# Kernel tuning notes

Measured on AMD Instinct MI355X. Metric: run time of the kernel, lower is better.

## Reference

```python
import jax, jax.numpy as jnp
import numpy as np

ALPHA = 0.5  # mixing weight between dot-product and wedge-norm terms


def setup_inputs() -> dict:
    key = jax.random.key(0)
    kq, kk, kv = jax.random.split(key, 3)
    B, L, H, E = 2, 2048, 8, 32
    queries = jax.random.normal(kq, (B, L, H, E), dtype=jnp.float32)
    keys = jax.random.normal(kk, (B, L, H, E), dtype=jnp.float32)
    values = jax.random.normal(kv, (B, L, H, E), dtype=jnp.float32)
    return {"queries": queries, "keys": keys, "values": values}


def reference(queries, keys, values):
    # queries: [B,L,H,E], keys: [B,S,H,E], values: [B,S,H,D]
    E = queries.shape[-1]
    scale = 1.0 / jnp.sqrt(jnp.asarray(E, dtype=queries.dtype))
    # dot product scores: [B,H,L,S]
    dot = jnp.einsum('blhe,bshe->bhls', queries, keys)
    # squared norms -> broadcastable [B,H,L,1] and [B,H,1,S]
    qn2 = jnp.sum(queries ** 2, axis=-1).transpose(0, 2, 1)[..., :, None]
    kn2 = jnp.sum(keys ** 2, axis=-1).transpose(0, 2, 1)[..., None, :]
    # wedge (Clifford) squared norm, clamped at 0
    wedge = jax.nn.relu(qn2 * kn2 - dot ** 2)
    scores = (ALPHA * dot - (1.0 - ALPHA) * wedge) * scale
    attn = jax.nn.softmax(scores, axis=-1)  # [B,H,L,S]
    # out: [B,L,H,D]
    out = jnp.einsum('bhls,bshd->blhd', attn, values)
    return out
```

## Files before the change

### kernel.cpp

```cpp
#include <hip/hip_runtime.h>
#include <hip/hip_bf16.h>
#include <math.h>


#define NB 2
#define NL 2048
#define NS 2048
#define NH 8
#define NBH 16
#define STRIPS 2
#define NT 16
#define CSC 0.12751742f
#define DEFER_THR 24.0f

#define WS_KN2_OFF 0u
#define WS_KHKL_OFF 131072u
#define WS_VT_OFF (131072u + 4194304u)
#define WS_PACC_OFF (131072u + 4194304u + 2097152u)
#define WS_PML_OFF (WS_PACC_OFF + 8388608u)
#define WS_NEED (WS_PML_OFF + 524288u)

typedef float f32x4 __attribute__((ext_vector_type(4)));
typedef float f32x2 __attribute__((ext_vector_type(2)));
typedef short s16x8 __attribute__((ext_vector_type(8)));
typedef unsigned short u16;

__device__ inline unsigned pk2(float a, float b) {
    __hip_bfloat162 t = __float22bfloat162_rn(make_float2(a, b));
    union { __hip_bfloat162 h; unsigned u; } cv;
    cv.h = t;
    return cv.u;
}
template <int CTRL>
__device__ inline float dpp_add(float x) {
    return x + __int_as_float(__builtin_amdgcn_mov_dpp(__float_as_int(x), CTRL, 0xF, 0xF, false));
}
__device__ inline void dma16(const void* gp, void* lp) {
    __builtin_amdgcn_global_load_lds(
        (__attribute__((address_space(1))) void*)(void*)gp,
        (__attribute__((address_space(3))) void*)lp, 16, 0, 0);
}
__device__ inline void pl32(unsigned& a, unsigned& b) {
    asm("v_permlane32_swap_b32 %0, %1" : "+v"(a), "+v"(b));
}
__device__ inline void pl16(unsigned& a, unsigned& b) {
    asm("v_permlane16_swap_b32 %0, %1" : "+v"(a), "+v"(b));
}
__device__ inline int swzK(int row) { return (row ^ (row >> 2)) & 3; }
__device__ inline int swzV(int row) { return (row + (row >> 3)) & 7; }

__global__ __launch_bounds__(256) void ga_pre(const float* __restrict__ K,
                                              const float* __restrict__ V,
                                              float* __restrict__ kn2w,
                                              u16* __restrict__ khkl,
                                              u16* __restrict__ vtw) {
    __shared__ float Vf[64][36];
    const int T = threadIdx.x;
    const int bh = blockIdx.x >> 5, stile = blockIdx.x & 31;
    const int b = bh >> 3, h = bh & 7;
    const int s0 = stile * 64;
    const int sk = T >> 2, kc = T & 3;

    const float* kp = K + ((size_t)((b * NS + s0 + sk) * NH + h)) * 32 + kc * 8;
    float4 f0 = *(const float4*)kp, f1 = *(const float4*)(kp + 4);
    float kx[8] = {f0.x, f0.y, f0.z, f0.w, f1.x, f1.y, f1.z, f1.w};
    unsigned hh[4], ll[4];
    float kn2p = 0.f;
#pragma unroll
    for (int i = 0; i < 4; i++) {
        float x0 = kx[2 * i], x1 = kx[2 * i + 1];
        kn2p = fmaf(x0, x0, kn2p);
        kn2p = fmaf(x1, x1, kn2p);
        unsigned h01 = pk2(x0, x1);
        hh[i] = h01;
        float h0 = __uint_as_float(h01 << 16);
        float h1 = __uint_as_float(h01 & 0xffff0000u);
        ll[i] = pk2(x0 - h0, x1 - h1);
    }
    u16* kd = khkl + ((size_t)(bh * NS + s0 + sk)) * 64;
    const int swk = sk & 7;
    *(uint4*)(kd + ((kc ^ swk) * 8)) = make_uint4(hh[0], hh[1], hh[2], hh[3]);
    *(uint4*)(kd + (((4 + kc) ^ swk) * 8)) = make_uint4(ll[0], ll[1], ll[2], ll[3]);
    kn2p = dpp_add<0xB1>(kn2p);
    kn2p = dpp_add<0x4E>(kn2p);
    if (kc == 0) kn2w[bh * NS + s0 + sk] = kn2p;

    const float* vp = V + ((size_t)((b * NS + s0 + sk) * NH + h)) * 32 + kc * 8;
    float4 g0 = *(const float4*)vp, g1 = *(const float4*)(vp + 4);
    const int chv = kc ^ ((sk >> 3) & 3);
    *(float4*)&Vf[sk][chv * 8] = g0;
    *(float4*)&Vf[sk][chv * 8 + 4] = g1;
    __syncthreads();
    const int dr = T >> 3, c = T & 7;
    float vv[8];
#pragma unroll
    for (int i = 0; i < 8; i++)
        vv[i] = Vf[c * 8 + i][(((dr >> 3) ^ (c & 3)) << 3) + (dr & 7)];
    const int phys = c ^ (dr & 7);
    *(uint4*)(vtw + ((size_t)(bh * 32 + dr)) * NS + s0 + phys * 8) =
        make_uint4(pk2(vv[0], vv[1]), pk2(vv[2], vv[3]), pk2(vv[4], vv[5]), pk2(vv[6], vv[7]));
}

__global__ __launch_bounds__(256, 3) void ga_dma(
    const float* __restrict__ Q, const float* __restrict__ kn2w,
    const u16* __restrict__ khkl, const u16* __restrict__ vtw,
    float* __restrict__ pacc, float* __restrict__ pml) {
    __shared__ u16 sK[2][64][64];
    __shared__ u16 sV[2][32][64];

    const int T = threadIdx.x;
    const int lane = T & 63, wave = T >> 6;
    const int g = lane >> 4, lc = lane & 15, g8 = g * 8;
    const int blk = blockIdx.x;
    const int qt = blk & 31, strip = (blk >> 5) & 1, bh = blk >> 6;
    const int b = bh >> 3, h = bh & 7;
    const int qw = qt * 64 + wave * 16;
    const int kb0 = strip * 1024;

    const float* qrow = Q + ((size_t)((b * NL + qw + lc) * NH + h)) * 32 + g8;
    float4 qa = *(const float4*)qrow, qb = *(const float4*)(qrow + 4);
    float q8[8] = {qa.x, qa.y, qa.z, qa.w, qb.x, qb.y, qb.z, qb.w};
    union { unsigned u4[4]; s16x8 v; } qh_, ql_;
    float qn2 = 0.f;
#pragma unroll
    for (int i = 0; i < 4; i++) {
        float x0 = q8[2 * i], x1 = q8[2 * i + 1];
        qn2 = fmaf(x0, x0, qn2);
        qn2 = fmaf(x1, x1, qn2);
        unsigned h01 = pk2(x0, x1);
        qh_.u4[i] = h01;
        float h0 = __uint_as_float(h01 << 16);
        float h1 = __uint_as_float(h01 & 0xffff0000u);
        ql_.u4[i] = pk2(x0 - h0, x1 - h1);
    }
    const s16x8 qh = qh_.v, ql = ql_.v;
    qn2 += __shfl_xor(qn2, 16);
    qn2 += __shfl_xor(qn2, 32);

    const char* ksrc = (const char*)khkl +
        ((size_t)(bh * NS + kb0 + 16 * wave)) * 128 + lane * 16;
    const char* vsrc = (const char*)vtw +
        ((size_t)(bh * 32 + 8 * wave + (lane >> 3))) * (NS * 2) +
        (size_t)(kb0 + (lane & 7) * 8) * 2;
    const float* kn2b = kn2w + (size_t)bh * NS + kb0;

    dma16(ksrc, &sK[0][16 * wave][0]);
    dma16(ksrc + 1024, &sK[0][16 * wave + 8][0]);
    dma16(vsrc, &sV[0][8 * wave][0]);
    __syncthreads();

    s16x8 ones;
#pragma unroll
    for (int i = 0; i < 8; i++) ones[i] = (short)0x3F80;

    f32x4 acc0 = {0.f, 0.f, 0.f, 0.f}, acc1 = {0.f, 0.f, 0.f, 0.f};
    f32x4 lacc = {0.f, 0.f, 0.f, 0.f};
    float m = -1e30f;
    const f32x4 z = {0.f, 0.f, 0.f, 0.f};
    const int sw = lc & 7;

    f32x4 d_p[4], kn2_p[4];
    s16x8 va_p[4];

    auto frags_qk = [&](int buf, f32x4* dc) {
#pragma unroll
        for (int st = 0; st < 4; st++) {
            s16x8 kh = *(s16x8*)&sK[buf][16 * st + lc][(g ^ sw) * 8];
            s16x8 klo = *(s16x8*)&sK[buf][16 * st + lc][((4 + g) ^ sw) * 8];
            f32x4 dd = __builtin_amdgcn_mfma_f32_16x16x32_bf16(klo, qh, z, 0, 0, 0);
            dd = __builtin_amdgcn_mfma_f32_16x16x32_bf16(kh, ql, dd, 0, 0, 0);
            dd = __builtin_amdgcn_mfma_f32_16x16x32_bf16(kh, qh, dd, 0, 0, 0);
            dc[st] = dd;
        }
    };
    auto load_v = [&](int buf, s16x8* va) {
        va[0] = *(s16x8*)&sV[buf][lc][(g ^ sw) * 8];
        va[1] = *(s16x8*)&sV[buf][lc][((4 + g) ^ sw) * 8];
        va[2] = *(s16x8*)&sV[buf][lc + 16][(g ^ sw) * 8];
        va[3] = *(s16x8*)&sV[buf][lc + 16][((4 + g) ^ sw) * 8];
    };
    auto softmax_pv = [&](const f32x4* dp, const f32x4* kn2p, const s16x8* vap) {
        const f32x2 qn2v = {qn2, qn2};
        float sc[4][4];
#pragma unroll
        for (int st = 0; st < 4; st++) {
            f32x2 dd0 = {dp[st][0], dp[st][1]}, dd1 = {dp[st][2], dp[st][3]};
            f32x2 kk0 = {kn2p[st][0], kn2p[st][1]}, kk1 = {kn2p[st][2], kn2p[st][3]};
            f32x2 e0 = dd0 - qn2v * kk0;
            f32x2 e1 = dd1 - qn2v * kk1;
            f32x2 t0 = dd0 * dd0 + e0;
            f32x2 t1 = dd1 * dd1 + e1;
            sc[st][0] = fminf(dp[st][0], t0[0]);
            sc[st][1] = fminf(dp[st][1], t0[1]);
            sc[st][2] = fminf(dp[st][2], t1[0]);
            sc[st][3] = fminf(dp[st][3], t1[1]);
        }
        float a0 = fmaxf(fmaxf(sc[0][0], sc[0][1]), sc[0][2]);
        float a1 = fmaxf(fmaxf(sc[0][3], sc[1][0]), sc[1][1]);
        float a2 = fmaxf(fmaxf(sc[1][2], sc[1][3]), sc[2][0]);
        float a3 = fmaxf(fmaxf(sc[2][1], sc[2][2]), sc[2][3]);
        float a4 = fmaxf(fmaxf(sc[3][0], sc[3][1]), sc[3][2]);
        float tm = fmaxf(fmaxf(fmaxf(a0, a1), fmaxf(a2, a3)), fmaxf(a4, sc[3][3]));
        if (!__all(tm <= m + DEFER_THR)) {
            tm = fmaxf(tm, __shfl_xor(tm, 16));
            tm = fmaxf(tm, __shfl_xor(tm, 32));
            const float nm = fmaxf(m, tm);
            const float al = __builtin_amdgcn_exp2f((m - nm) * CSC);
            m = nm;
            acc0 *= al;
            acc1 *= al;
            lacc *= al;
        }
        const float negmC = -m * CSC;
        const f32x2 cscv = {CSC, CSC}, nmv = {negmC, negmC};
        float p[4][4];
#pragma unroll
        for (int st = 0; st < 4; st++) {
            f32x2 s0 = {sc[st][0], sc[st][1]}, s1 = {sc[st][2], sc[st][3]};
            f32x2 e0 = s0 * cscv + nmv;
            f32x2 e1 = s1 * cscv + nmv;
            p[st][0] = __builtin_amdgcn_exp2f(e0[0]);
            p[st][1] = __builtin_amdgcn_exp2f(e0[1]);
            p[st][2] = __builtin_amdgcn_exp2f(e1[0]);
            p[st][3] = __builtin_amdgcn_exp2f(e1[1]);
        }
        unsigned w00 = pk2(p[0][0], p[0][1]), w01 = pk2(p[0][2], p[0][3]);
        unsigned w10 = pk2(p[1][0], p[1][1]), w11 = pk2(p[1][2], p[1][3]);
        unsigned w20 = pk2(p[2][0], p[2][1]), w21 = pk2(p[2][2], p[2][3]);
        unsigned w30 = pk2(p[3][0], p[3][1]), w31 = pk2(p[3][2], p[3][3]);
        pl32(w00, w10); pl32(w01, w11);
        pl16(w00, w10); pl16(w01, w11);
        pl32(w20, w30); pl32(w21, w31);
        pl16(w20, w30); pl16(w21, w31);
        union { uint4 u; s16x8 v; } Pb0, Pb1;
        Pb0.u = make_uint4(w00, w01, w10, w11);
        Pb1.u = make_uint4(w20, w21, w30, w31);
        const s16x8 pb0 = Pb0.v, pb1 = Pb1.v;
        acc0 = __builtin_amdgcn_mfma_f32_16x16x32_bf16(vap[0], pb0, acc0, 0, 0, 0);
        acc0 = __builtin_amdgcn_mfma_f32_16x16x32_bf16(vap[1], pb1, acc0, 0, 0, 0);
        acc1 = __builtin_amdgcn_mfma_f32_16x16x32_bf16(vap[2], pb0, acc1, 0, 0, 0);
        acc1 = __builtin_amdgcn_mfma_f32_16x16x32_bf16(vap[3], pb1, acc1, 0, 0, 0);
        lacc = __builtin_amdgcn_mfma_f32_16x16x32_bf16(ones, pb0, lacc, 0, 0, 0);
        lacc = __builtin_amdgcn_mfma_f32_16x16x32_bf16(ones, pb1, lacc, 0, 0, 0);
    };

    {
        dma16(ksrc + 8192, &sK[1][16 * wave][0]);
        dma16(ksrc + 8192 + 1024, &sK[1][16 * wave + 8][0]);
        dma16(vsrc + 128, &sV[1][8 * wave][0]);
        frags_qk(0, d_p);
#pragma unroll
        for (int st = 0; st < 4; st++)
            kn2_p[st] = *(const f32x4*)(kn2b + 16 * st + 4 * g);
        load_v(0, va_p);
        __syncthreads();
    }

#pragma unroll 2
    for (int i = 1; i < NT; ++i) {
        const int cur = i & 1;
        if (i + 1 < NT) {
            const char* k2 = ksrc + (size_t)(i + 1) * 8192;
            const char* v2 = vsrc + (size_t)(i + 1) * 128;
            dma16(k2, &sK[cur ^ 1][16 * wave][0]);
            dma16(k2 + 1024, &sK[cur ^ 1][16 * wave + 8][0]);
            dma16(v2, &sV[cur ^ 1][8 * wave][0]);
        }
        f32x4 d_c[4], kn2_c[4];
        frags_qk(cur, d_c);
#pragma unroll
        for (int st = 0; st < 4; st++)
            kn2_c[st] = *(const f32x4*)(kn2b + i * 64 + 16 * st + 4 * g);
        softmax_pv(d_p, kn2_p, va_p);
        s16x8 va_c[4];
        load_v(cur, va_c);
#pragma unroll
        for (int st = 0; st < 4; st++) {
            d_p[st] = d_c[st];
            kn2_p[st] = kn2_c[st];
            va_p[st] = va_c[st];
        }
        if (i + 1 < NT) __syncthreads();
    }
    softmax_pv(d_p, kn2_p, va_p);

    const float l = lacc[0];
    float* pa = pacc + (((size_t)bh * STRIPS + strip) * NL + (qw + lc)) * 32;
    *(f32x4*)(pa + 4 * g) = acc0;
    *(f32x4*)(pa + 16 + 4 * g) = acc1;
    if (g == 0) {
        *(float2*)(pml + (((size_t)bh * STRIPS + strip) * NL + (qw + lc)) * 2) =
            make_float2(m, l);
    }
}

__global__ __launch_bounds__(256) void ga_combine(const float* __restrict__ pacc,
                                                  const float* __restrict__ pml,
                                                  float* __restrict__ O) {
    const int tid = blockIdx.x * 256 + threadIdx.x;
    const int dq = tid & 7, q = (tid >> 3) & 2047, bh = tid >> 14;
    const int b = bh >> 3, h = bh & 7;
    float2 t0 = *(const float2*)(pml + (((size_t)bh * STRIPS + 0) * NL + q) * 2);
    float2 t1 = *(const float2*)(pml + (((size_t)bh * STRIPS + 1) * NL + q) * 2);
    const float mf = fmaxf(t0.x, t1.x);
    float w0 = __builtin_amdgcn_exp2f((t0.x - mf) * CSC);
    float w1 = __builtin_amdgcn_exp2f((t1.x - mf) * CSC);
    const float inv = 1.f / fmaf(t0.y, w0, t1.y * w1);
    w0 *= inv;
    w1 *= inv;
    const float* pa0 = pacc + (((size_t)bh * STRIPS + 0) * NL + q) * 32 + dq * 4;
    const float* pa1 = pacc + (((size_t)bh * STRIPS + 1) * NL + q) * 32 + dq * 4;
    float4 a0 = *(const float4*)pa0, a1 = *(const float4*)pa1;
    float4 o;
    o.x = fmaf(a0.x, w0, a1.x * w1);
    o.y = fmaf(a0.y, w0, a1.y * w1);
    o.z = fmaf(a0.z, w0, a1.z * w1);
    o.w = fmaf(a0.w, w0, a1.w * w1);
    *(float4*)(O + (((size_t)(b * NL + q)) * NH + h) * 32 + dq * 4) = o;
}

__global__ __launch_bounds__(512, 4) void ga_fallback(
    const float* __restrict__ Q, const float* __restrict__ K,
    const float* __restrict__ V, float* __restrict__ O) {
    __shared__ union {
        struct {
            u16 Kh[2][64][32];
            u16 Kl[2][64][32];
            u16 Vt[2][32][64];
            float kn2[2][64];
        } s;
        struct { float acc[8][32][17]; float m[8][16]; float l[8][16]; } c;
    } u;
    __shared__ u16 sP[8][16][64];

    const int T = threadIdx.x;
    const int lane = T & 63, wave = T >> 6;
    const int g = lane >> 4, lc = lane & 15, g8 = g * 8;
    const int half = wave >> 2;
    const int qt = blockIdx.x & 31;
    const int bh = blockIdx.x >> 5;
    const int b = bh >> 3, h = bh & 7;
    const int qw = qt * 64 + (wave & 3) * 16;

    const float* qrow = Q + ((size_t)((b * NL + qw + lc) * NH + h)) * 32 + g8;
    float4 qa = *(const float4*)qrow, qb = *(const float4*)(qrow + 4);
    float q8[8] = {qa.x, qa.y, qa.z, qa.w, qb.x, qb.y, qb.z, qb.w};
    union { unsigned u4[4]; s16x8 v; } qh_, ql_;
    float qn2 = 0.f;
#pragma unroll
    for (int i = 0; i < 4; i++) {
        float x0 = q8[2 * i], x1 = q8[2 * i + 1];
        qn2 = fmaf(x0, x0, qn2);
        qn2 = fmaf(x1, x1, qn2);
        unsigned h01 = pk2(x0, x1);
        qh_.u4[i] = h01;
        float h0 = __uint_as_float(h01 << 16);
        float h1 = __uint_as_float(h01 & 0xffff0000u);
        ql_.u4[i] = pk2(x0 - h0, x1 - h1);
    }
    const s16x8 qh = qh_.v, ql = ql_.v;
    qn2 += __shfl_xor(qn2, 16);
    qn2 += __shfl_xor(qn2, 32);

    const int Tl = T & 255;
    const int sk = Tl >> 2, kc = Tl & 3;
    const int dv = Tl & 31, vc = Tl >> 5;
    const float* kbase = K + ((size_t)(b * NS * NH) + h) * 32;
    const float* vbase = V + ((size_t)(b * NS * NH) + h) * 32;
    const int kphys = (kc ^ swzK(sk)) * 8;
    const int vphys = (vc ^ swzV(dv)) * 8;

    int s0 = half * 1024;
    float4 ka = *(const float4*)(kbase + (size_t)(s0 + sk) * 256 + kc * 8);
    float4 kb = *(const float4*)(kbase + (size_t)(s0 + sk) * 256 + kc * 8 + 4);
    float vr[8];
#pragma unroll
    for (int i = 0; i < 8; i++) vr[i] = vbase[(size_t)(s0 + 8 * vc + i) * 256 + dv];

    f32x4 acc0 = {0.f, 0.f, 0.f, 0.f}, acc1 = {0.f, 0.f, 0.f, 0.f};
    float m = -INFINITY, l = 0.f;

    for (int t = 0; t < 16; ++t) {
        {
            float kx[8] = {ka.x, ka.y, ka.z, ka.w, kb.x, kb.y, kb.z, kb.w};
            unsigned hh[4], ll[4];
            float kn2p = 0.f;
#pragma unroll
            for (int i = 0; i < 4; i++) {
                float x0 = kx[2 * i], x1 = kx[2 * i + 1];
                kn2p = fmaf(x0, x0, kn2p);
                kn2p = fmaf(x1, x1, kn2p);
                unsigned h01 = pk2(x0, x1);
                hh[i] = h01;
                float h0 = __uint_as_float(h01 << 16);
                float h1 = __uint_as_float(h01 & 0xffff0000u);
                ll[i] = pk2(x0 - h0, x1 - h1);
            }
            *(uint4*)&u.s.Kh[half][sk][kphys] = make_uint4(hh[0], hh[1], hh[2], hh[3]);
            *(uint4*)&u.s.Kl[half][sk][kphys] = make_uint4(ll[0], ll[1], ll[2], ll[3]);
            kn2p = dpp_add<0xB1>(kn2p);
            kn2p = dpp_add<0x4E>(kn2p);
            if (kc == 0) u.s.kn2[half][sk] = kn2p;
            *(uint4*)&u.s.Vt[half][dv][vphys] =
                make_uint4(pk2(vr[0], vr[1]), pk2(vr[2], vr[3]),
                           pk2(vr[4], vr[5]), pk2(vr[6], vr[7]));
        }
        const int tn = (t + 1 < 16) ? t + 1 : t;
        const int sn = half * 1024 + tn * 64;
        ka = *(const float4*)(kbase + (size_t)(sn + sk) * 256 + kc * 8);
        kb = *(const float4*)(kbase + (size_t)(sn + sk) * 256 + kc * 8 + 4);
#pragma unroll
        for (int i = 0; i < 8; i++) vr[i] = vbase[(size_t)(sn + 8 * vc + i) * 256 + dv];

        __syncthreads();

        f32x4 d[4], kn2v[4];
        const f32x4 z = {0.f, 0.f, 0.f, 0.f};
        const int skr = swzK(lc);
#pragma unroll
        for (int st = 0; st < 4; st++) {
            kn2v[st] = *(f32x4*)&u.s.kn2[half][16 * st + 4 * g];
            s16x8 kh = *(s16x8*)&u.s.Kh[half][16 * st + lc][(g ^ skr) * 8];
            s16x8 kl = *(s16x8*)&u.s.Kl[half][16 * st + lc][(g ^ skr) * 8];
            f32x4 dd = __builtin_amdgcn_mfma_f32_16x16x32_bf16(kl, qh, z, 0, 0, 0);
            dd = __builtin_amdgcn_mfma_f32_16x16x32_bf16(kh, ql, dd, 0, 0, 0);
            dd = __builtin_amdgcn_mfma_f32_16x16x32_bf16(kh, qh, dd, 0, 0, 0);
            d[st] = dd;
        }

        float sc[4][4];
#pragma unroll
        for (int st = 0; st < 4; st++)
#pragma unroll
            for (int r = 0; r < 4; r++) {
                float dd = d[st][r];
                float w = fmaxf(fmaf(-dd, dd, qn2 * kn2v[st][r]), 0.f);
                sc[st][r] = (dd - w) * CSC;
            }

        float x0 = fmaxf(fmaxf(sc[0][0], sc[0][1]), fmaxf(sc[0][2], sc[0][3]));
        float x1 = fmaxf(fmaxf(sc[1][0], sc[1][1]), fmaxf(sc[1][2], sc[1][3]));
        float x2 = fmaxf(fmaxf(sc[2][0], sc[2][1]), fmaxf(sc[2][2], sc[2][3]));
        float x3 = fmaxf(fmaxf(sc[3][0], sc[3][1]), fmaxf(sc[3][2], sc[3][3]));
        float tm = fmaxf(fmaxf(x0, x1), fmaxf(x2, x3));
        tm = fmaxf(tm, __shfl_xor(tm, 16));
        tm = fmaxf(tm, __shfl_xor(tm, 32));
        const float nm = fmaxf(m, tm);
        const float al = __builtin_amdgcn_exp2f(m - nm);
        m = nm;
        float p[4][4], ls = 0.f;
#pragma unroll
        for (int st = 0; st < 4; st++)
#pragma unroll
            for (int r = 0; r < 4; r++) {
                p[st][r] = __builtin_amdgcn_exp2f(sc[st][r] - nm);
                ls += p[st][r];
            }
        l = fmaf(l, al, ls);
        acc0 *= al;
        acc1 *= al;

#pragma unroll
        for (int st = 0; st < 4; st++) {
            const int off = ((2 * st + (g >> 1)) ^ (lc & 7)) * 8 + (g & 1) * 4;
            *(uint2*)&sP[wave][lc][off] =
                make_uint2(pk2(p[st][0], p[st][1]), pk2(p[st][2], p[st][3]));
        }
        __builtin_amdgcn_s_waitcnt(0xC07F);

        const int svl = swzV(lc), svh = swzV(lc + 16), spl = lc & 7;
        s16x8 va00 = *(s16x8*)&u.s.Vt[half][lc][(g ^ svl) * 8];
        s16x8 va01 = *(s16x8*)&u.s.Vt[half][lc][((4 + g) ^ svl) * 8];
        s16x8 va10 = *(s16x8*)&u.s.Vt[half][lc + 16][(g ^ svh) * 8];
        s16x8 va11 = *(s16x8*)&u.s.Vt[half][lc + 16][((4 + g) ^ svh) * 8];
        s16x8 pb0 = *(s16x8*)&sP[wave][lc][(g ^ spl) * 8];
        s16x8 pb1 = *(s16x8*)&sP[wave][lc][((4 + g) ^ spl) * 8];
        acc0 = __builtin_amdgcn_mfma_f32_16x16x32_bf16(va00, pb0, acc0, 0, 0, 0);
        acc0 = __builtin_amdgcn_mfma_f32_16x16x32_bf16(va01, pb1, acc0, 0, 0, 0);
        acc1 = __builtin_amdgcn_mfma_f32_16x16x32_bf16(va10, pb0, acc1, 0, 0, 0);
        acc1 = __builtin_amdgcn_mfma_f32_16x16x32_bf16(va11, pb1, acc1, 0, 0, 0);

        __syncthreads();
    }

    l += __shfl_xor(l, 16);
    l += __shfl_xor(l, 32);
#pragma unroll
    for (int r = 0; r < 4; r++) {
        u.c.acc[wave][4 * g + r][lc] = acc0[r];
        u.c.acc[wave][16 + 4 * g + r][lc] = acc1[r];
    }
    if (lane < 16) {
        u.c.m[wave][lc] = m;
        u.c.l[wave][lc] = l;
    }
    __syncthreads();

    const int q = T >> 3, dq = (T & 7) * 4, qr = q & 15;
    const int w0 = q >> 4, w1 = w0 + 4;
    float m0 = u.c.m[w0][qr], m1 = u.c.m[w1][qr];
    float l0 = u.c.l[w0][qr], l1 = u.c.l[w1][qr];
    float mf = fmaxf(m0, m1);
    float e0 = __builtin_amdgcn_exp2f(m0 - mf);
    float e1 = __builtin_amdgcn_exp2f(m1 - mf);
    float inv = 1.f / fmaf(l1, e1, l0 * e0);
    e0 *= inv;
    e1 *= inv;
    float4 o;
    o.x = u.c.acc[w0][dq + 0][qr] * e0 + u.c.acc[w1][dq + 0][qr] * e1;
    o.y = u.c.acc[w0][dq + 1][qr] * e0 + u.c.acc[w1][dq + 1][qr] * e1;
    o.z = u.c.acc[w0][dq + 2][qr] * e0 + u.c.acc[w1][dq + 2][qr] * e1;
    o.w = u.c.acc[w0][dq + 3][qr] * e0 + u.c.acc[w1][dq + 3][qr] * e1;
    *(float4*)(O + ((size_t)((b * NL + qt * 64 + q) * NH + h)) * 32 + dq) = o;
}

extern "C" void kernel_launch(void* const* d_in, const int* in_sizes, int n_in,
                              void* d_out, int out_size, void* d_ws, size_t ws_size,
                              hipStream_t stream) {
    const float* Q = (const float*)d_in[0];
    const float* K = (const float*)d_in[1];
    const float* V = (const float*)d_in[2];
    float* O = (float*)d_out;

    if (ws_size >= (size_t)WS_NEED) {
        float* kn2w = (float*)((char*)d_ws + WS_KN2_OFF);
        u16* khkl = (u16*)((char*)d_ws + WS_KHKL_OFF);
        u16* vtw = (u16*)((char*)d_ws + WS_VT_OFF);
        float* pacc = (float*)((char*)d_ws + WS_PACC_OFF);
        float* pml = (float*)((char*)d_ws + WS_PML_OFF);
        ga_pre<<<NBH * 32, 256, 0, stream>>>(K, V, kn2w, khkl, vtw);
        ga_dma<<<NBH * 32 * STRIPS, 256, 0, stream>>>(Q, kn2w, khkl, vtw, pacc, pml);
        ga_combine<<<(NBH * NL * 8) / 256, 256, 0, stream>>>(pacc, pml, O);
    } else {
        ga_fallback<<<NBH * 32, 512, 0, stream>>>(Q, K, V, O);
    }
}
```

Baseline: 106.4 us.

## Load K/V fragments directly from global into registers instead of LDS DMA

```diff
diff --git a/kernel.cpp b/kernel.cpp
--- a/kernel.cpp
+++ b/kernel.cpp
@@ -34,11 +34,6 @@
 template <int CTRL>
 __device__ inline float dpp_add(float x) {
     return x + __int_as_float(__builtin_amdgcn_mov_dpp(__float_as_int(x), CTRL, 0xF, 0xF, false));
-}
-__device__ inline void dma16(const void* gp, void* lp) {
-    __builtin_amdgcn_global_load_lds(
-        (__attribute__((address_space(1))) void*)(void*)gp,
-        (__attribute__((address_space(3))) void*)lp, 16, 0, 0);
 }
 __device__ inline void pl32(unsigned& a, unsigned& b) {
     asm("v_permlane32_swap_b32 %0, %1" : "+v"(a), "+v"(b));
@@ -78,9 +73,8 @@
         ll[i] = pk2(x0 - h0, x1 - h1);
     }
     u16* kd = khkl + ((size_t)(bh * NS + s0 + sk)) * 64;
-    const int swk = sk & 7;
-    *(uint4*)(kd + ((kc ^ swk) * 8)) = make_uint4(hh[0], hh[1], hh[2], hh[3]);
-    *(uint4*)(kd + (((4 + kc) ^ swk) * 8)) = make_uint4(ll[0], ll[1], ll[2], ll[3]);
+    *(uint4*)(kd + kc * 8) = make_uint4(hh[0], hh[1], hh[2], hh[3]);
+    *(uint4*)(kd + (4 + kc) * 8) = make_uint4(ll[0], ll[1], ll[2], ll[3]);
     kn2p = dpp_add<0xB1>(kn2p);
     kn2p = dpp_add<0x4E>(kn2p);
     if (kc == 0) kn2w[bh * NS + s0 + sk] = kn2p;
@@ -96,23 +90,20 @@
 #pragma unroll
     for (int i = 0; i < 8; i++)
         vv[i] = Vf[c * 8 + i][(((dr >> 3) ^ (c & 3)) << 3) + (dr & 7)];
-    const int phys = c ^ (dr & 7);
-    *(uint4*)(vtw + ((size_t)(bh * 32 + dr)) * NS + s0 + phys * 8) =
+    *(uint4*)(vtw + ((size_t)(bh * 32 + dr)) * NS + s0 + c * 8) =
         make_uint4(pk2(vv[0], vv[1]), pk2(vv[2], vv[3]), pk2(vv[4], vv[5]), pk2(vv[6], vv[7]));
 }
 
-__global__ __launch_bounds__(256, 3) void ga_dma(
+__global__ __launch_bounds__(256, 3) void ga_reg(
     const float* __restrict__ Q, const float* __restrict__ kn2w,
     const u16* __restrict__ khkl, const u16* __restrict__ vtw,
     float* __restrict__ pacc, float* __restrict__ pml) {
-    __shared__ u16 sK[2][64][64];
-    __shared__ u16 sV[2][32][64];
-
     const int T = threadIdx.x;
     const int lane = T & 63, wave = T >> 6;
     const int g = lane >> 4, lc = lane & 15, g8 = g * 8;
     const int blk = blockIdx.x;
-    const int qt = blk & 31, strip = (blk >> 5) & 1, bh = blk >> 6;
+    const int grp = blk & 31, qt = blk >> 5;
+    const int bh = grp >> 1, strip = grp & 1;
     const int b = bh >> 3, h = bh & 7;
     const int qw = qt * 64 + wave * 16;
     const int kb0 = strip * 1024;
@@ -137,17 +128,9 @@
     qn2 += __shfl_xor(qn2, 16);
     qn2 += __shfl_xor(qn2, 32);
 
-    const char* ksrc = (const char*)khkl +
-        ((size_t)(bh * NS + kb0 + 16 * wave)) * 128 + lane * 16;
-    const char* vsrc = (const char*)vtw +
-        ((size_t)(bh * 32 + 8 * wave + (lane >> 3))) * (NS * 2) +
-        (size_t)(kb0 + (lane & 7) * 8) * 2;
-    const float* kn2b = kn2w + (size_t)bh * NS + kb0;
-
-    dma16(ksrc, &sK[0][16 * wave][0]);
-    dma16(ksrc + 1024, &sK[0][16 * wave + 8][0]);
-    dma16(vsrc, &sV[0][8 * wave][0]);
-    __syncthreads();
+    const u16* kbase = khkl + ((size_t)(bh * NS + kb0) + lc) * 64 + g8;
+    const u16* vbase = vtw + ((size_t)(bh * 32 + lc)) * NS + kb0 + g8;
+    const float* kn2b = kn2w + (size_t)bh * NS + kb0 + 4 * g;
 
     s16x8 ones;
 #pragma unroll
@@ -157,44 +140,61 @@
     f32x4 lacc = {0.f, 0.f, 0.f, 0.f};
     float m = -1e30f;
     const f32x4 z = {0.f, 0.f, 0.f, 0.f};
-    const int sw = lc & 7;
-
-    f32x4 d_p[4], kn2_p[4];
-    s16x8 va_p[4];
-
-    auto frags_qk = [&](int buf, f32x4* dc) {
+
+    for (int t = 0; t < NT; ++t) {
+        const u16* kt = kbase + t * (64 * 64);
+        const u16* vt = vbase + t * 64;
+        const float* knt = kn2b + t * 64;
+        s16x8 kh0 = *(const s16x8*)(kt);
+        s16x8 kl0 = *(const s16x8*)(kt + 32);
+        s16x8 kh1 = *(const s16x8*)(kt + 16 * 64);
+        s16x8 kl1 = *(const s16x8*)(kt + 16 * 64 + 32);
+        s16x8 kh2 = *(const s16x8*)(kt + 32 * 64);
+        s16x8 kl2 = *(const s16x8*)(kt + 32 * 64 + 32);
+        s16x8 kh3 = *(const s16x8*)(kt + 48 * 64);
+        s16x8 kl3 = *(const s16x8*)(kt + 48 * 64 + 32);
+        s16x8 va0 = *(const s16x8*)(vt);
+        s16x8 va1 = *(const s16x8*)(vt + 32);
+        s16x8 va2 = *(const s16x8*)(vt + 16 * NS);
+        s16x8 va3 = *(const s16x8*)(vt + 16 * NS + 32);
+        f32x4 kn2v0 = *(const f32x4*)(knt);
+        f32x4 kn2v1 = *(const f32x4*)(knt + 16);
+        f32x4 kn2v2 = *(const f32x4*)(knt + 32);
+        f32x4 kn2v3 = *(const f32x4*)(knt + 48);
+
+        f32x4 d[4];
+        {
+            f32x4 dd = __builtin_amdgcn_mfma_f32_16x16x32_bf16(kl0, qh, z, 0, 0, 0);
+            dd = __builtin_amdgcn_mfma_f32_16x16x32_bf16(kh0, ql, dd, 0, 0, 0);
+            d[0] = __builtin_amdgcn_mfma_f32_16x16x32_bf16(kh0, qh, dd, 0, 0, 0);
+            dd = __builtin_amdgcn_mfma_f32_16x16x32_bf16(kl1, qh, z, 0, 0, 0);
+            dd = __builtin_amdgcn_mfma_f32_16x16x32_bf16(kh1, ql, dd, 0, 0, 0);
+            d[1] = __builtin_amdgcn_mfma_f32_16x16x32_bf16(kh1, qh, dd, 0, 0, 0);
+            dd = __builtin_amdgcn_mfma_f32_16x16x32_bf16(kl2, qh, z, 0, 0, 0);
+            dd = __builtin_amdgcn_mfma_f32_16x16x32_bf16(kh2, ql, dd, 0, 0, 0);
+            d[2] = __builtin_amdgcn_mfma_f32_16x16x32_bf16(kh2, qh, dd, 0, 0, 0);
+            dd = __builtin_amdgcn_mfma_f32_16x16x32_bf16(kl3, qh, z, 0, 0, 0);
+            dd = __builtin_amdgcn_mfma_f32_16x16x32_bf16(kh3, ql, dd, 0, 0, 0);
+            d[3] = __builtin_amdgcn_mfma_f32_16x16x32_bf16(kh3, qh, dd, 0, 0, 0);
+        }
+
+        const f32x2 qn2v = {qn2, qn2};
+        f32x4 kn2m[4] = {kn2v0, kn2v1, kn2v2, kn2v3};
+        float sc[4][4];
 #pragma unroll
         for (int st = 0; st < 4; st++) {
-            s16x8 kh = *(s16x8*)&sK[buf][16 * st + lc][(g ^ sw) * 8];
-            s16x8 klo = *(s16x8*)&sK[buf][16 * st + lc][((4 + g) ^ sw) * 8];
-            f32x4 dd = __builtin_amdgcn_mfma_f32_16x16x32_bf16(klo, qh, z, 0, 0, 0);
-            dd = __builtin_amdgcn_mfma_f32_16x16x32_bf16(kh, ql, dd, 0, 0, 0);
-            dd = __builtin_amdgcn_mfma_f32_16x16x32_bf16(kh, qh, dd, 0, 0, 0);
-            dc[st] = dd;
-        }
-    };
-    auto load_v = [&](int buf, s16x8* va) {
-        va[0] = *(s16x8*)&sV[buf][lc][(g ^ sw) * 8];
-        va[1] = *(s16x8*)&sV[buf][lc][((4 + g) ^ sw) * 8];
-        va[2] = *(s16x8*)&sV[buf][lc + 16][(g ^ sw) * 8];
-        va[3] = *(s16x8*)&sV[buf][lc + 16][((4 + g) ^ sw) * 8];
-    };
-    auto softmax_pv = [&](const f32x4* dp, const f32x4* kn2p, const s16x8* vap) {
-        const f32x2 qn2v = {qn2, qn2};
-        float sc[4][4];
-#pragma unroll
-        for (int st = 0; st < 4; st++) {
-            f32x2 dd0 = {dp[st][0], dp[st][1]}, dd1 = {dp[st][2], dp[st][3]};
-            f32x2 kk0 = {kn2p[st][0], kn2p[st][1]}, kk1 = {kn2p[st][2], kn2p[st][3]};
+            f32x2 dd0 = {d[st][0], d[st][1]}, dd1 = {d[st][2], d[st][3]};
+            f32x2 kk0 = {kn2m[st][0], kn2m[st][1]}, kk1 = {kn2m[st][2], kn2m[st][3]};
             f32x2 e0 = dd0 - qn2v * kk0;
             f32x2 e1 = dd1 - qn2v * kk1;
             f32x2 t0 = dd0 * dd0 + e0;
             f32x2 t1 = dd1 * dd1 + e1;
-            sc[st][0] = fminf(dp[st][0], t0[0]);
-            sc[st][1] = fminf(dp[st][1], t0[1]);
-            sc[st][2] = fminf(dp[st][2], t1[0]);
-            sc[st][3] = fminf(dp[st][3], t1[1]);
-        }
+            sc[st][0] = fminf(d[st][0], t0[0]);
+            sc[st][1] = fminf(d[st][1], t0[1]);
+            sc[st][2] = fminf(d[st][2], t1[0]);
+            sc[st][3] = fminf(d[st][3], t1[1]);
+        }
+
         float a0 = fmaxf(fmaxf(sc[0][0], sc[0][1]), sc[0][2]);
         float a1 = fmaxf(fmaxf(sc[0][3], sc[1][0]), sc[1][1]);
         float a2 = fmaxf(fmaxf(sc[1][2], sc[1][3]), sc[2][0]);
@@ -224,6 +224,7 @@
             p[st][2] = __builtin_amdgcn_exp2f(e1[0]);
             p[st][3] = __builtin_amdgcn_exp2f(e1[1]);
         }
+
         unsigned w00 = pk2(p[0][0], p[0][1]), w01 = pk2(p[0][2], p[0][3]);
         unsigned w10 = pk2(p[1][0], p[1][1]), w11 = pk2(p[1][2], p[1][3]);
         unsigned w20 = pk2(p[2][0], p[2][1]), w21 = pk2(p[2][2], p[2][3]);
@@ -236,53 +237,14 @@
         Pb0.u = make_uint4(w00, w01, w10, w11);
         Pb1.u = make_uint4(w20, w21, w30, w31);
         const s16x8 pb0 = Pb0.v, pb1 = Pb1.v;
-        acc0 = __builtin_amdgcn_mfma_f32_16x16x32_bf16(vap[0], pb0, acc0, 0, 0, 0);
-        acc0 = __builtin_amdgcn_mfma_f32_16x16x32_bf16(vap[1], pb1, acc0, 0, 0, 0);
-        acc1 = __builtin_amdgcn_mfma_f32_16x16x32_bf16(vap[2], pb0, acc1, 0, 0, 0);
-        acc1 = __builtin_amdgcn_mfma_f32_16x16x32_bf16(vap[3], pb1, acc1, 0, 0, 0);
+
+        acc0 = __builtin_amdgcn_mfma_f32_16x16x32_bf16(va0, pb0, acc0, 0, 0, 0);
+        acc0 = __builtin_amdgcn_mfma_f32_16x16x32_bf16(va1, pb1, acc0, 0, 0, 0);
+        acc1 = __builtin_amdgcn_mfma_f32_16x16x32_bf16(va2, pb0, acc1, 0, 0, 0);
+        acc1 = __builtin_amdgcn_mfma_f32_16x16x32_bf16(va3, pb1, acc1, 0, 0, 0);
         lacc = __builtin_amdgcn_mfma_f32_16x16x32_bf16(ones, pb0, lacc, 0, 0, 0);
         lacc = __builtin_amdgcn_mfma_f32_16x16x32_bf16(ones, pb1, lacc, 0, 0, 0);
-    };
-
-    {
-        dma16(ksrc + 8192, &sK[1][16 * wave][0]);
-        dma16(ksrc + 8192 + 1024, &sK[1][16 * wave + 8][0]);
-        dma16(vsrc + 128, &sV[1][8 * wave][0]);
-        frags_qk(0, d_p);
-#pragma unroll
-        for (int st = 0; st < 4; st++)
-            kn2_p[st] = *(const f32x4*)(kn2b + 16 * st + 4 * g);
-        load_v(0, va_p);
-        __syncthreads();
-    }
-
-#pragma unroll 2
-    for (int i = 1; i < NT; ++i) {
-        const int cur = i & 1;
-        if (i + 1 < NT) {
-            const char* k2 = ksrc + (size_t)(i + 1) * 8192;
-            const char* v2 = vsrc + (size_t)(i + 1) * 128;
-            dma16(k2, &sK[cur ^ 1][16 * wave][0]);
-            dma16(k2 + 1024, &sK[cur ^ 1][16 * wave + 8][0]);
-            dma16(v2, &sV[cur ^ 1][8 * wave][0]);
-        }
-        f32x4 d_c[4], kn2_c[4];
-        frags_qk(cur, d_c);
-#pragma unroll
-        for (int st = 0; st < 4; st++)
-            kn2_c[st] = *(const f32x4*)(kn2b + i * 64 + 16 * st + 4 * g);
-        softmax_pv(d_p, kn2_p, va_p);
-        s16x8 va_c[4];
-        load_v(cur, va_c);
-#pragma unroll
-        for (int st = 0; st < 4; st++) {
-            d_p[st] = d_c[st];
-            kn2_p[st] = kn2_c[st];
-            va_p[st] = va_c[st];
-        }
-        if (i + 1 < NT) __syncthreads();
-    }
-    softmax_pv(d_p, kn2_p, va_p);
+    }
 
     const float l = lacc[0];
     float* pa = pacc + (((size_t)bh * STRIPS + strip) * NL + (qw + lc)) * 32;
@@ -529,7 +491,7 @@
         float* pacc = (float*)((char*)d_ws + WS_PACC_OFF);
         float* pml = (float*)((char*)d_ws + WS_PML_OFF);
         ga_pre<<<NBH * 32, 256, 0, stream>>>(K, V, kn2w, khkl, vtw);
-        ga_dma<<<NBH * 32 * STRIPS, 256, 0, stream>>>(Q, kn2w, khkl, vtw, pacc, pml);
+        ga_reg<<<NBH * 32 * STRIPS, 256, 0, stream>>>(Q, kn2w, khkl, vtw, pacc, pml);
         ga_combine<<<(NBH * NL * 8) / 256, 256, 0, stream>>>(pacc, pml, O);
     } else {
         ga_fallback<<<NBH * 32, 512, 0, stream>>>(Q, K, V, O);
```

Measured after the change: 163.3 us. 53.5% more time.
